# Kernel tuning notes

Hardware: AMD Instinct MI355X
Metric: run time of the kernel (lower is better)

The kernel has to match this reference:

```python
import jax, jax.numpy as jnp
import numpy as np

B, S, D, H = 8, 1024, 1024, 16
DH = D // H  # per-head dim = 64
SCALE = float(np.sqrt(DH))  # normalize_coeff = sqrt(dim_h_k)


def _ln(x, g, b, eps=1e-5):
    m = jnp.mean(x, axis=-1, keepdims=True)
    v = jnp.mean(jnp.square(x - m), axis=-1, keepdims=True)
    return (x - m) / jnp.sqrt(v + eps) * g + b


def setup_inputs() -> dict:
    key = jax.random.key(0)
    ks = jax.random.split(key, 12)
    w = lambda k, shape: (jax.random.normal(k, shape, dtype=jnp.float32) * 0.02)
    return {
        "X": jax.random.normal(ks[0], (B, S, D), dtype=jnp.float32),
        # stacked per-head projection weights (torch Linear: y = x @ W.T + b -> store as [H, D, DH])
        "Wq": w(ks[1], (H, D, DH)), "bq": jnp.zeros((H, DH), jnp.float32),
        "Wk": w(ks[2], (H, D, DH)), "bk": jnp.zeros((H, DH), jnp.float32),
        "Wv": w(ks[3], (H, D, DH)), "bv": jnp.zeros((H, DH), jnp.float32),
        "pre_g": jnp.ones((D,), jnp.float32), "pre_b": jnp.zeros((D,), jnp.float32),
        "post_g": jnp.ones((D,), jnp.float32), "post_b": jnp.zeros((D,), jnp.float32),
        "W1": w(ks[4], (D, 2 * D)), "b1": jnp.zeros((2 * D,), jnp.float32),
        "ln1_g": jnp.ones((2 * D,), jnp.float32), "ln1_b": jnp.zeros((2 * D,), jnp.float32),
        "W2": w(ks[5], (2 * D, D)), "b2": jnp.zeros((D,), jnp.float32),
        "ln2_g": jnp.ones((D,), jnp.float32), "ln2_b": jnp.zeros((D,), jnp.float32),
    }


def reference(X, Wq, bq, Wk, bk, Wv, bv, pre_g, pre_b, post_g, post_b,
              W1, b1, ln1_g, ln1_b, W2, b2, ln2_g, ln2_b):
    # pre-LN + multi-head attention (all heads batched instead of python loop)
    t = _ln(X, pre_g, pre_b)
    q = jnp.einsum('bsd,hdk->bhsk', t, Wq) + bq[:, None, :]   # [B,H,S,DH]
    k = jnp.einsum('bsd,hdk->bhsk', t, Wk) + bk[:, None, :]
    v = jnp.einsum('bsd,hdk->bhsk', t, Wv) + bv[:, None, :]
    scores = jnp.einsum('bhqd,bhkd->bhqk', q, k) / SCALE       # [B,H,S,S]
    p = jax.nn.softmax(scores, axis=-1)
    o = jnp.einsum('bhqk,bhkd->bhqd', p, v)                    # [B,H,S,DH]
    o = o.transpose(0, 2, 1, 3).reshape(B, S, D)               # concat heads
    X = X + o
    # post-LN + MLP (Linear -> LN -> GELU -> Linear -> LN -> GELU)
    t2 = _ln(X, post_g, post_b)
    h = jax.nn.gelu(_ln(t2 @ W1 + b1, ln1_g, ln1_b), approximate=False)
    h = jax.nn.gelu(_ln(h @ W2 + b2, ln2_g, ln2_b), approximate=False)
    return X + h
```

## Files before the change

kernel.cpp:

```cpp
#include <hip/hip_runtime.h>

typedef __attribute__((ext_vector_type(8))) short s16x8;
typedef __attribute__((ext_vector_type(8))) unsigned short u16x8;
typedef __attribute__((ext_vector_type(4))) unsigned short u16x4;
typedef __attribute__((ext_vector_type(4))) float f32x4;

__device__ __forceinline__ unsigned short f2bf(float f) {
  union { float f; unsigned int u; } v; v.f = f;
  unsigned int r = (v.u + 0x7FFFu + ((v.u >> 16) & 1u)) >> 16;
  return (unsigned short)r;
}
__device__ __forceinline__ float bf2f(unsigned short h) {
  union { unsigned int u; float f; } v; v.u = ((unsigned int)h) << 16;
  return v.f;
}
__device__ __forceinline__ float gelu(float x) {
  return 0.5f * x * (1.f + erff(x * 0.70710678118654752f));
}
__device__ __forceinline__ float fexp2(float x) {
  float r; asm("v_exp_f32 %0, %1" : "=v"(r) : "v"(x)); return r;
}

__device__ __forceinline__ void gld16(const void* g, void* l) {
  __builtin_amdgcn_global_load_lds(
      (const __attribute__((address_space(1))) unsigned int*)g,
      (__attribute__((address_space(3))) unsigned int*)l, 16, 0, 0);
}

__device__ __forceinline__ float blk_sum(float v, float* red, int tid, int nw) {
#pragma unroll
  for (int m = 32; m >= 1; m >>= 1) v += __shfl_xor(v, m);
  __syncthreads();
  if ((tid & 63) == 0) red[tid >> 6] = v;
  __syncthreads();
  float t = 0.f;
  for (int i = 0; i < nw; ++i) t += red[i];
  return t;
}

__global__ __launch_bounds__(256) void k_tr(
    const float* __restrict__ in, unsigned short* __restrict__ out,
    int inRS, int outRS, long inBS, long outBS) {
  __shared__ float t[32][33];
  const float* ip = in + (size_t)blockIdx.z * inBS;
  unsigned short* op = out + (size_t)blockIdx.z * outBS;
  const int r0 = blockIdx.y * 32, c0 = blockIdx.x * 32;
  const int tid = threadIdx.x;
  const int r = tid >> 3, c4 = (tid & 7) * 4;
  const f32x4 v = *(const f32x4*)(ip + (size_t)(r0 + r) * inRS + c0 + c4);
#pragma unroll
  for (int i = 0; i < 4; ++i) t[r][c4 + i] = v[i];
  __syncthreads();
  u16x4 o;
#pragma unroll
  for (int i = 0; i < 4; ++i) o[i] = f2bf(t[c4 + i][r]);
  *(u16x4*)(op + (size_t)(c0 + r) * outRS + r0 + c4) = o;
}

__global__ __launch_bounds__(256) void k_bias3(
    const float* __restrict__ a, const float* __restrict__ b,
    const float* __restrict__ c, float* __restrict__ o) {
  int i = blockIdx.x * 256 + threadIdx.x;
  if (i >= 3072) return;
  o[i] = (i < 1024) ? a[i] : ((i < 2048) ? b[i - 1024] : c[i - 2048]);
}

__global__ __launch_bounds__(256) void k_pre_ln(
    const float* __restrict__ X, const float* __restrict__ g,
    const float* __restrict__ bta, unsigned short* __restrict__ out) {
  __shared__ float red[4];
  const int row = blockIdx.x, tid = threadIdx.x;
  const f32x4 x = *(const f32x4*)(X + (size_t)row * 1024 + tid * 4);
  float s = x[0] + x[1] + x[2] + x[3];
  s = blk_sum(s, red, tid, 4);
  const float mean = s * (1.f / 1024.f);
  f32x4 d;
#pragma unroll
  for (int i = 0; i < 4; ++i) d[i] = x[i] - mean;
  float sq = d[0] * d[0] + d[1] * d[1] + d[2] * d[2] + d[3] * d[3];
  sq = blk_sum(sq, red, tid, 4);
  const float rstd = rsqrtf(sq * (1.f / 1024.f) + 1e-5f);
  const f32x4 gv = *(const f32x4*)(g + tid * 4);
  const f32x4 bv = *(const f32x4*)(bta + tid * 4);
  u16x4 o;
#pragma unroll
  for (int i = 0; i < 4; ++i) o[i] = f2bf(d[i] * rstd * gv[i] + bv[i]);
  *(u16x4*)(out + (size_t)row * 1024 + tid * 4) = o;
}

__global__ __launch_bounds__(256) void k_res_ln(
    const float* __restrict__ X, const unsigned short* __restrict__ attn,
    const float* __restrict__ g, const float* __restrict__ bta,
    float* __restrict__ X1, unsigned short* __restrict__ t2) {
  __shared__ float red[4];
  const int row = blockIdx.x, tid = threadIdx.x;
  const f32x4 x = *(const f32x4*)(X + (size_t)row * 1024 + tid * 4);
  const u16x4 a = *(const u16x4*)(attn + (size_t)row * 1024 + tid * 4);
  f32x4 x1;
#pragma unroll
  for (int i = 0; i < 4; ++i) x1[i] = x[i] + bf2f(a[i]);
  *(f32x4*)(X1 + (size_t)row * 1024 + tid * 4) = x1;
  float s = x1[0] + x1[1] + x1[2] + x1[3];
  s = blk_sum(s, red, tid, 4);
  const float mean = s * (1.f / 1024.f);
  f32x4 d;
#pragma unroll
  for (int i = 0; i < 4; ++i) d[i] = x1[i] - mean;
  float sq = d[0] * d[0] + d[1] * d[1] + d[2] * d[2] + d[3] * d[3];
  sq = blk_sum(sq, red, tid, 4);
  const float rstd = rsqrtf(sq * (1.f / 1024.f) + 1e-5f);
  const f32x4 gv = *(const f32x4*)(g + tid * 4);
  const f32x4 bv = *(const f32x4*)(bta + tid * 4);
  u16x4 o;
#pragma unroll
  for (int i = 0; i < 4; ++i) o[i] = f2bf(d[i] * rstd * gv[i] + bv[i]);
  *(u16x4*)(t2 + (size_t)row * 1024 + tid * 4) = o;
}

__global__ __launch_bounds__(256) void k_ln_gelu(
    const unsigned short* __restrict__ in, const float* __restrict__ g,
    const float* __restrict__ bta, unsigned short* __restrict__ out) {
  __shared__ float red[4];
  const int row = blockIdx.x, tid = threadIdx.x;
  const u16x8 iv = *(const u16x8*)(in + (size_t)row * 2048 + tid * 8);
  float v[8];
  float s = 0.f;
#pragma unroll
  for (int i = 0; i < 8; ++i) { v[i] = bf2f(iv[i]); s += v[i]; }
  s = blk_sum(s, red, tid, 4);
  const float mean = s * (1.f / 2048.f);
  float sq = 0.f;
#pragma unroll
  for (int i = 0; i < 8; ++i) { v[i] -= mean; sq += v[i] * v[i]; }
  sq = blk_sum(sq, red, tid, 4);
  const float rstd = rsqrtf(sq * (1.f / 2048.f) + 1e-5f);
  u16x8 o;
#pragma unroll
  for (int i = 0; i < 8; ++i) {
    float t = v[i] * rstd * g[tid * 8 + i] + bta[tid * 8 + i];
    o[i] = f2bf(gelu(t));
  }
  *(u16x8*)(out + (size_t)row * 2048 + tid * 8) = o;
}

__global__ __launch_bounds__(256) void k_final(
    const unsigned short* __restrict__ in, const float* __restrict__ g,
    const float* __restrict__ bta, float* __restrict__ io) {
  __shared__ float red[4];
  const int row = blockIdx.x, tid = threadIdx.x;
  const u16x4 iv = *(const u16x4*)(in + (size_t)row * 1024 + tid * 4);
  float v[4];
  float s = 0.f;
#pragma unroll
  for (int i = 0; i < 4; ++i) { v[i] = bf2f(iv[i]); s += v[i]; }
  s = blk_sum(s, red, tid, 4);
  const float mean = s * (1.f / 1024.f);
  float sq = 0.f;
#pragma unroll
  for (int i = 0; i < 4; ++i) { v[i] -= mean; sq += v[i] * v[i]; }
  sq = blk_sum(sq, red, tid, 4);
  const float rstd = rsqrtf(sq * (1.f / 1024.f) + 1e-5f);
  const f32x4 gv = *(const f32x4*)(g + tid * 4);
  const f32x4 bv = *(const f32x4*)(bta + tid * 4);
  f32x4 xi = *(const f32x4*)(io + (size_t)row * 1024 + tid * 4);
#pragma unroll
  for (int i = 0; i < 4; ++i)
    xi[i] += gelu(v[i] * rstd * gv[i] + bv[i]);
  *(f32x4*)(io + (size_t)row * 1024 + tid * 4) = xi;
}

__global__ __launch_bounds__(256) void k_gemm(
    const unsigned short* __restrict__ A, const unsigned short* __restrict__ Bt,
    const float* __restrict__ bias, unsigned short* __restrict__ C,
    int M, int N, int K, int vsplit, unsigned short* __restrict__ VtO) {
  __shared__ __align__(16) unsigned short As[128 * 64];
  __shared__ __align__(16) unsigned short Bs[128 * 64];
  const int tid = threadIdx.x;
  const int w = tid >> 6, l = tid & 63;
  const int gx = gridDim.x;
  int flat = blockIdx.y * gx + blockIdx.x;
  const int nwg = gx * gridDim.y;
  if ((nwg & 7) == 0) flat = (flat & 7) * (nwg >> 3) + (flat >> 3);
  const int m0 = (flat / gx) * 128, n0 = (flat % gx) * 128;
  const int wr = (w >> 1) * 64, wc = (w & 1) * 64;
  const f32x4 z4 = {0.f, 0.f, 0.f, 0.f};
  f32x4 acc[4][4];
#pragma unroll
  for (int i = 0; i < 4; ++i)
#pragma unroll
    for (int j = 0; j < 4; ++j) acc[i][j] = z4;

  const int srow = l >> 3, scol = (l & 7) * 8;
  for (int kt = 0; kt < K; kt += 64) {
#pragma unroll
    for (int i = 0; i < 4; ++i) {
      const int u = i * 4 + w;
      const int row = u * 8 + srow;
      gld16(A + (size_t)(m0 + row) * K + kt + scol, As + u * 512 + l * 8);
      gld16(Bt + (size_t)(n0 + row) * K + kt + scol, Bs + u * 512 + l * 8);
    }
    __syncthreads();
#pragma unroll
    for (int ks = 0; ks < 2; ++ks) {
      const int kb = ks * 32 + (l >> 4) * 8;
      s16x8 a[4], b[4];
#pragma unroll
      for (int m = 0; m < 4; ++m)
        a[m] = *(const s16x8*)(As + (wr + m * 16 + (l & 15)) * 64 + kb);
#pragma unroll
      for (int n = 0; n < 4; ++n)
        b[n] = *(const s16x8*)(Bs + (wc + n * 16 + (l & 15)) * 64 + kb);
#pragma unroll
      for (int m = 0; m < 4; ++m)
#pragma unroll
        for (int n = 0; n < 4; ++n)
          acc[m][n] = __builtin_amdgcn_mfma_f32_16x16x32_bf16(a[m], b[n], acc[m][n], 0, 0, 0);
    }
    __syncthreads();
  }
  const int rbase = m0 + wr + ((l >> 4) << 2);
  const int cbase = n0 + wc + (l & 15);
#pragma unroll
  for (int n = 0; n < 4; ++n) {
    const int c = cbase + n * 16;
    const float bb = bias[c];
    if ((n0 + wc + n * 16) < vsplit) {
#pragma unroll
      for (int m = 0; m < 4; ++m)
#pragma unroll
        for (int r = 0; r < 4; ++r)
          C[(size_t)(rbase + m * 16 + r) * N + c] = f2bf(acc[m][n][r] + bb);
    } else {
      const int cc = c - vsplit;
      const int hh = cc >> 6, dd = cc & 63;
#pragma unroll
      for (int m = 0; m < 4; ++m) {
        const int rr = rbase + m * 16;
        u16x4 o;
#pragma unroll
        for (int r = 0; r < 4; ++r) o[r] = f2bf(acc[m][n][r] + bb);
        *(u16x4*)(VtO + ((size_t)((rr >> 10) * 16 + hh)) * 65536 + dd * 1024 + (rr & 1023)) = o;
      }
    }
  }
}

__device__ __forceinline__ int swz(int r, int c) {
  return r * 64 + (c ^ ((r & 7) << 3));
}

__global__ __launch_bounds__(256) void k_attn3(
    const unsigned short* __restrict__ qkv, const unsigned short* __restrict__ Vt,
    unsigned short* __restrict__ O) {
  int bid = blockIdx.x;
  bid = (bid & 7) * 256 + (bid >> 3);
  const int qt = bid & 15, h = (bid >> 4) & 15, b = bid >> 8;
  const int tid = threadIdx.x, w = tid >> 6, l = tid & 63;
  const int arow = l & 15, kcol = (l >> 4) * 8;

  __shared__ __align__(16) unsigned short Kb[2][64 * 64];
  __shared__ __align__(16) unsigned short Vb[2][64 * 64];
  __shared__ __align__(16) unsigned short Ps[4][16 * 64];
  unsigned short* ps = &Ps[w][0];

  const unsigned short* qb = qkv + (size_t)b * 1024 * 3072 + h * 64;
  const unsigned short* kb = qb + 1024;
  const unsigned short* vt = Vt + ((size_t)(b * 16 + h)) * 65536;
  const int q0 = qt * 64 + w * 16;

  s16x8 qa[2];
#pragma unroll
  for (int kh = 0; kh < 2; ++kh)
    qa[kh] = *(const s16x8*)(qb + (size_t)(q0 + arow) * 3072 + kh * 32 + kcol);

  const int srow = tid >> 3;
  const int sce = 8 * ((tid & 7) ^ (srow & 7));
  const int sdst = srow * 64 + (tid & 7) * 8;

#pragma unroll
  for (int i = 0; i < 2; ++i) {
    gld16(kb + (size_t)(i * 32 + srow) * 3072 + sce, Kb[0] + i * 2048 + sdst);
    gld16(vt + (size_t)(i * 32 + srow) * 1024 + sce, Vb[0] + i * 2048 + sdst);
  }
  __syncthreads();

  const f32x4 z4 = {0.f, 0.f, 0.f, 0.f};
  f32x4 oacc[4];
#pragma unroll
  for (int i = 0; i < 4; ++i) oacc[i] = z4;
  float mrun[4], lrun[4];
#pragma unroll
  for (int r = 0; r < 4; ++r) { mrun[r] = -1e30f; lrun[r] = 0.f; }

  const float c2 = 0.125f * 1.44269504088896f;

  for (int kc = 0; kc < 16; ++kc) {
    const int cur = kc & 1;
    if (kc < 15) {
      const int key1 = (kc + 1) * 64;
#pragma unroll
      for (int i = 0; i < 2; ++i) {
        gld16(kb + (size_t)(key1 + i * 32 + srow) * 3072 + sce, Kb[cur ^ 1] + i * 2048 + sdst);
        gld16(vt + (size_t)(i * 32 + srow) * 1024 + key1 + sce, Vb[cur ^ 1] + i * 2048 + sdst);
      }
    }
    f32x4 sacc[4];
#pragma unroll
    for (int t = 0; t < 4; ++t) {
      s16x8 k0 = *(const s16x8*)(Kb[cur] + swz(t * 16 + arow, kcol));
      s16x8 k1 = *(const s16x8*)(Kb[cur] + swz(t * 16 + arow, 32 + kcol));
      f32x4 s = z4;
      s = __builtin_amdgcn_mfma_f32_16x16x32_bf16(qa[0], k0, s, 0, 0, 0);
      s = __builtin_amdgcn_mfma_f32_16x16x32_bf16(qa[1], k1, s, 0, 0, 0);
      sacc[t] = s;
    }
    float ss[4][4];
#pragma unroll
    for (int t = 0; t < 4; ++t)
#pragma unroll
      for (int r = 0; r < 4; ++r) ss[t][r] = sacc[t][r] * c2;

    float nm[4], sc[4], psum[4];
#pragma unroll
    for (int r = 0; r < 4; ++r) {
      float m = fmaxf(fmaxf(ss[0][r], ss[1][r]), fmaxf(ss[2][r], ss[3][r]));
#pragma unroll
      for (int msk = 8; msk >= 1; msk >>= 1) m = fmaxf(m, __shfl_xor(m, msk));
      nm[r] = fmaxf(mrun[r], m);
      sc[r] = fexp2(mrun[r] - nm[r]);
      mrun[r] = nm[r];
      psum[r] = 0.f;
    }
#pragma unroll
    for (int t = 0; t < 4; ++t)
#pragma unroll
      for (int r = 0; r < 4; ++r) {
        float p = fexp2(ss[t][r] - nm[r]);
        psum[r] += p;
        ps[swz(((l >> 4) << 2) + r, t * 16 + arow)] = f2bf(p);
      }
#pragma unroll
    for (int r = 0; r < 4; ++r) {
      float s = psum[r];
#pragma unroll
      for (int msk = 8; msk >= 1; msk >>= 1) s += __shfl_xor(s, msk);
      lrun[r] = lrun[r] * sc[r] + s;
#pragma unroll
      for (int dg = 0; dg < 4; ++dg) oacc[dg][r] *= sc[r];
    }
    s16x8 pa[2];
#pragma unroll
    for (int kh = 0; kh < 2; ++kh)
      pa[kh] = *(const s16x8*)(ps + swz(arow, kh * 32 + kcol));
#pragma unroll
    for (int dg = 0; dg < 4; ++dg) {
      s16x8 v0 = *(const s16x8*)(Vb[cur] + swz(dg * 16 + arow, kcol));
      s16x8 v1 = *(const s16x8*)(Vb[cur] + swz(dg * 16 + arow, 32 + kcol));
      oacc[dg] = __builtin_amdgcn_mfma_f32_16x16x32_bf16(pa[0], v0, oacc[dg], 0, 0, 0);
      oacc[dg] = __builtin_amdgcn_mfma_f32_16x16x32_bf16(pa[1], v1, oacc[dg], 0, 0, 0);
    }
    __syncthreads();
  }

  float inv[4];
#pragma unroll
  for (int r = 0; r < 4; ++r) inv[r] = 1.f / lrun[r];
#pragma unroll
  for (int dg = 0; dg < 4; ++dg)
#pragma unroll
    for (int r = 0; r < 4; ++r) {
      const int row = q0 + ((l >> 4) << 2) + r;
      O[(size_t)(b * 1024 + row) * 1024 + h * 64 + dg * 16 + arow] = f2bf(oacc[dg][r] * inv[r]);
    }
}

extern "C" void kernel_launch(void* const* d_in, const int* in_sizes, int n_in,
                              void* d_out, int out_size, void* d_ws, size_t ws_size,
                              hipStream_t stream) {
  const float* X = (const float*)d_in[0];
  const float* Wq = (const float*)d_in[1];
  const float* bq = (const float*)d_in[2];
  const float* Wk = (const float*)d_in[3];
  const float* bk = (const float*)d_in[4];
  const float* Wv = (const float*)d_in[5];
  const float* bv = (const float*)d_in[6];
  const float* pre_g = (const float*)d_in[7];
  const float* pre_b = (const float*)d_in[8];
  const float* post_g = (const float*)d_in[9];
  const float* post_b = (const float*)d_in[10];
  const float* W1 = (const float*)d_in[11];
  const float* b1 = (const float*)d_in[12];
  const float* ln1_g = (const float*)d_in[13];
  const float* ln1_b = (const float*)d_in[14];
  const float* W2 = (const float*)d_in[15];
  const float* b2 = (const float*)d_in[16];
  const float* ln2_g = (const float*)d_in[17];
  const float* ln2_b = (const float*)d_in[18];
  float* out = (float*)d_out;

  char* ws = (char*)d_ws;
  const size_t MB = (size_t)1 << 20;
  unsigned short* t_bf = (unsigned short*)(ws);
  unsigned short* attn_o = (unsigned short*)(ws);
  unsigned short* mlp2 = (unsigned short*)(ws);
  unsigned short* qkv = (unsigned short*)(ws + 16 * MB);
  unsigned short* mlp1 = (unsigned short*)(ws + 16 * MB);
  unsigned short* Vt = (unsigned short*)(ws + 64 * MB);
  unsigned short* h1 = (unsigned short*)(ws + 48 * MB);
  unsigned short* t2 = (unsigned short*)(ws + 80 * MB);
  unsigned short* Wqkvt = (unsigned short*)(ws + 96 * MB);
  unsigned short* W1t = (unsigned short*)(ws + 102 * MB);
  unsigned short* W2t = (unsigned short*)(ws + 106 * MB);
  float* biasq = (float*)(ws + 110 * MB);

  k_tr<<<dim3(2, 32, 16), 256, 0, stream>>>(Wq, Wqkvt, 64, 1024, 65536, 65536);
  k_tr<<<dim3(2, 32, 16), 256, 0, stream>>>(Wk, Wqkvt + 1048576, 64, 1024, 65536, 65536);
  k_tr<<<dim3(2, 32, 16), 256, 0, stream>>>(Wv, Wqkvt + 2097152, 64, 1024, 65536, 65536);
  k_tr<<<dim3(64, 32, 1), 256, 0, stream>>>(W1, W1t, 2048, 1024, 0, 0);
  k_tr<<<dim3(32, 64, 1), 256, 0, stream>>>(W2, W2t, 1024, 2048, 0, 0);
  k_bias3<<<12, 256, 0, stream>>>(bq, bk, bv, biasq);

  k_pre_ln<<<8192, 256, 0, stream>>>(X, pre_g, pre_b, t_bf);
  k_gemm<<<dim3(24, 64), 256, 0, stream>>>(t_bf, Wqkvt, biasq, qkv, 8192, 3072, 1024, 2048, Vt);
  k_attn3<<<2048, 256, 0, stream>>>(qkv, Vt, attn_o);
  k_res_ln<<<8192, 256, 0, stream>>>(X, attn_o, post_g, post_b, out, t2);
  k_gemm<<<dim3(16, 64), 256, 0, stream>>>(t2, W1t, b1, mlp1, 8192, 2048, 1024, 1 << 30, nullptr);
  k_ln_gelu<<<8192, 256, 0, stream>>>(mlp1, ln1_g, ln1_b, h1);
  k_gemm<<<dim3(8, 64), 256, 0, stream>>>(h1, W2t, b2, mlp2, 8192, 1024, 2048, 1 << 30, nullptr);
  k_final<<<8192, 256, 0, stream>>>(mlp2, ln2_g, ln2_b, out);
}
```

Before: 536.6 us.

## Triple-buffer swizzled 256x128 GEMM and streamline attention softmax bookkeeping

The GEMM becomes a 512-thread, 256x128-tile kernel with three-stage dynamic-LDS buffering. It issues loads two tiles ahead with explicit vmcnt waits, uses an XOR-swizzled LDS layout and raises wave priority around the MFMA block. The aim is to hide global-load latency, cut LDS bank conflicts and halve B-operand traffic per output. Attention folds the softmax scale into Q, computes the row sum via MFMA against a ones vector, and skips rescaling when the running max grows by 8 or less. These changes risk bf16 rounding of the scaled Q, and the large LDS use limits occupancy to one block per CU.

Result: faster. 519.1 us (-3.3%).

```diff
diff --git a/kernel.cpp b/kernel.cpp
--- a/kernel.cpp
+++ b/kernel.cpp
@@ -169,20 +169,20 @@
   *(f32x4*)(io + (size_t)row * 1024 + tid * 4) = xi;
 }
 
-__global__ __launch_bounds__(256) void k_gemm(
+__global__ __launch_bounds__(512) void k_gemm2(
     const unsigned short* __restrict__ A, const unsigned short* __restrict__ Bt,
     const float* __restrict__ bias, unsigned short* __restrict__ C,
     int M, int N, int K, int vsplit, unsigned short* __restrict__ VtO) {
-  __shared__ __align__(16) unsigned short As[128 * 64];
-  __shared__ __align__(16) unsigned short Bs[128 * 64];
+  extern __shared__ __align__(16) unsigned short lds[];
   const int tid = threadIdx.x;
   const int w = tid >> 6, l = tid & 63;
+  const int wm = w >> 1, wn = w & 1;
   const int gx = gridDim.x;
   int flat = blockIdx.y * gx + blockIdx.x;
   const int nwg = gx * gridDim.y;
   if ((nwg & 7) == 0) flat = (flat & 7) * (nwg >> 3) + (flat >> 3);
-  const int m0 = (flat / gx) * 128, n0 = (flat % gx) * 128;
-  const int wr = (w >> 1) * 64, wc = (w & 1) * 64;
+  const int m0 = (flat / gx) * 256, n0 = (flat % gx) * 128;
+
   const f32x4 z4 = {0.f, 0.f, 0.f, 0.f};
   f32x4 acc[4][4];
 #pragma unroll
@@ -190,41 +190,75 @@
 #pragma unroll
     for (int j = 0; j < 4; ++j) acc[i][j] = z4;
 
-  const int srow = l >> 3, scol = (l & 7) * 8;
-  for (int kt = 0; kt < K; kt += 64) {
-#pragma unroll
-    for (int i = 0; i < 4; ++i) {
-      const int u = i * 4 + w;
-      const int row = u * 8 + srow;
-      gld16(A + (size_t)(m0 + row) * K + kt + scol, As + u * 512 + l * 8);
-      gld16(Bt + (size_t)(n0 + row) * K + kt + scol, Bs + u * 512 + l * 8);
+#define STAGE_G2(t, d)                                                              \
+  {                                                                                 \
+    const int kb = (t) * 64;                                                        \
+    _Pragma("unroll") for (int i = 0; i < 4; ++i) {                                 \
+      const int s = i * 512 + tid;                                                  \
+      const int row = s >> 3, cs = s & 7;                                           \
+      gld16(A + (size_t)(m0 + row) * K + kb + ((cs ^ (row & 7)) << 3),              \
+            lds + (d) * 24576 + s * 8);                                             \
+    }                                                                               \
+    _Pragma("unroll") for (int i = 0; i < 2; ++i) {                                 \
+      const int s = i * 512 + tid;                                                  \
+      const int row = s >> 3, cs = s & 7;                                           \
+      gld16(Bt + (size_t)(n0 + row) * K + kb + ((cs ^ (row & 7)) << 3),             \
+            lds + (d) * 24576 + 16384 + s * 8);                                     \
+    }                                                                               \
+  }
+
+  const int nt = K >> 6;
+  STAGE_G2(0, 0);
+  STAGE_G2(1, 1);
+
+  for (int t = 0; t < nt; ++t) {
+    const int d = t % 3;
+    if (t + 2 < nt) {
+      const int d2 = (t + 2) % 3;
+      STAGE_G2(t + 2, d2);
+      asm volatile("s_waitcnt vmcnt(12)" ::: "memory");
+    } else if (t + 1 < nt) {
+      asm volatile("s_waitcnt vmcnt(6)" ::: "memory");
+    } else {
+      asm volatile("s_waitcnt vmcnt(0)" ::: "memory");
     }
     __syncthreads();
+
+    const unsigned short* Ab = lds + d * 24576;
+    const unsigned short* Bb = Ab + 16384;
+    __builtin_amdgcn_s_setprio(1);
 #pragma unroll
     for (int ks = 0; ks < 2; ++ks) {
-      const int kb = ks * 32 + (l >> 4) * 8;
+      const int cs = ks * 4 + (l >> 4);
       s16x8 a[4], b[4];
 #pragma unroll
-      for (int m = 0; m < 4; ++m)
-        a[m] = *(const s16x8*)(As + (wr + m * 16 + (l & 15)) * 64 + kb);
-#pragma unroll
-      for (int n = 0; n < 4; ++n)
-        b[n] = *(const s16x8*)(Bs + (wc + n * 16 + (l & 15)) * 64 + kb);
+      for (int m = 0; m < 4; ++m) {
+        const int row = wm * 64 + m * 16 + (l & 15);
+        a[m] = *(const s16x8*)(Ab + row * 64 + ((cs ^ (row & 7)) << 3));
+      }
+#pragma unroll
+      for (int n = 0; n < 4; ++n) {
+        const int row = wn * 64 + n * 16 + (l & 15);
+        b[n] = *(const s16x8*)(Bb + row * 64 + ((cs ^ (row & 7)) << 3));
+      }
 #pragma unroll
       for (int m = 0; m < 4; ++m)
 #pragma unroll
         for (int n = 0; n < 4; ++n)
           acc[m][n] = __builtin_amdgcn_mfma_f32_16x16x32_bf16(a[m], b[n], acc[m][n], 0, 0, 0);
     }
+    __builtin_amdgcn_s_setprio(0);
     __syncthreads();
   }
-  const int rbase = m0 + wr + ((l >> 4) << 2);
-  const int cbase = n0 + wc + (l & 15);
+#undef STAGE_G2
+
+  const int rbase = m0 + wm * 64 + ((l >> 4) << 2);
+  const int cbase = n0 + wn * 64 + (l & 15);
 #pragma unroll
   for (int n = 0; n < 4; ++n) {
     const int c = cbase + n * 16;
     const float bb = bias[c];
-    if ((n0 + wc + n * 16) < vsplit) {
+    if ((n0 + wn * 64 + n * 16) < vsplit) {
 #pragma unroll
       for (int m = 0; m < 4; ++m)
 #pragma unroll
@@ -268,10 +302,20 @@
   const unsigned short* vt = Vt + ((size_t)(b * 16 + h)) * 65536;
   const int q0 = qt * 64 + w * 16;
 
+  const float c2 = 0.125f * 1.44269504088896f;
+
   s16x8 qa[2];
 #pragma unroll
-  for (int kh = 0; kh < 2; ++kh)
-    qa[kh] = *(const s16x8*)(qb + (size_t)(q0 + arow) * 3072 + kh * 32 + kcol);
+  for (int kh = 0; kh < 2; ++kh) {
+    s16x8 q = *(const s16x8*)(qb + (size_t)(q0 + arow) * 3072 + kh * 32 + kcol);
+#pragma unroll
+    for (int j = 0; j < 8; ++j)
+      q[j] = (short)f2bf(bf2f((unsigned short)q[j]) * c2);
+    qa[kh] = q;
+  }
+  s16x8 ones;
+#pragma unroll
+  for (int j = 0; j < 8; ++j) ones[j] = (short)0x3F80;
 
   const int srow = tid >> 3;
   const int sce = 8 * ((tid & 7) ^ (srow & 7));
@@ -288,11 +332,10 @@
   f32x4 oacc[4];
 #pragma unroll
   for (int i = 0; i < 4; ++i) oacc[i] = z4;
-  float mrun[4], lrun[4];
-#pragma unroll
-  for (int r = 0; r < 4; ++r) { mrun[r] = -1e30f; lrun[r] = 0.f; }
-
-  const float c2 = 0.125f * 1.44269504088896f;
+  f32x4 lacc = z4;
+  float mrun[4];
+#pragma unroll
+  for (int r = 0; r < 4; ++r) mrun[r] = -1e30f;
 
   for (int kc = 0; kc < 16; ++kc) {
     const int cur = kc & 1;
@@ -314,44 +357,44 @@
       s = __builtin_amdgcn_mfma_f32_16x16x32_bf16(qa[1], k1, s, 0, 0, 0);
       sacc[t] = s;
     }
-    float ss[4][4];
+    float rmax[4];
+#pragma unroll
+    for (int r = 0; r < 4; ++r) {
+      float m = fmaxf(fmaxf(sacc[0][r], sacc[1][r]), fmaxf(sacc[2][r], sacc[3][r]));
+#pragma unroll
+      for (int msk = 8; msk >= 1; msk >>= 1) m = fmaxf(m, __shfl_xor(m, msk));
+      rmax[r] = m;
+    }
+    const float need = fmaxf(fmaxf(rmax[0] - mrun[0], rmax[1] - mrun[1]),
+                             fmaxf(rmax[2] - mrun[2], rmax[3] - mrun[3]));
+    if (!__all(need <= 8.f)) {
+      float sc[4];
+#pragma unroll
+      for (int r = 0; r < 4; ++r) {
+        const float nm = fmaxf(mrun[r], rmax[r]);
+        sc[r] = fexp2(mrun[r] - nm);
+        mrun[r] = nm;
+      }
+#pragma unroll
+      for (int r = 0; r < 4; ++r) {
+        lacc[r] *= sc[r];
+#pragma unroll
+        for (int dg = 0; dg < 4; ++dg) oacc[dg][r] *= sc[r];
+      }
+    }
 #pragma unroll
     for (int t = 0; t < 4; ++t)
 #pragma unroll
-      for (int r = 0; r < 4; ++r) ss[t][r] = sacc[t][r] * c2;
-
-    float nm[4], sc[4], psum[4];
-#pragma unroll
-    for (int r = 0; r < 4; ++r) {
-      float m = fmaxf(fmaxf(ss[0][r], ss[1][r]), fmaxf(ss[2][r], ss[3][r]));
-#pragma unroll
-      for (int msk = 8; msk >= 1; msk >>= 1) m = fmaxf(m, __shfl_xor(m, msk));
-      nm[r] = fmaxf(mrun[r], m);
-      sc[r] = fexp2(mrun[r] - nm[r]);
-      mrun[r] = nm[r];
-      psum[r] = 0.f;
-    }
-#pragma unroll
-    for (int t = 0; t < 4; ++t)
-#pragma unroll
       for (int r = 0; r < 4; ++r) {
-        float p = fexp2(ss[t][r] - nm[r]);
-        psum[r] += p;
+        const float p = fexp2(sacc[t][r] - mrun[r]);
         ps[swz(((l >> 4) << 2) + r, t * 16 + arow)] = f2bf(p);
       }
-#pragma unroll
-    for (int r = 0; r < 4; ++r) {
-      float s = psum[r];
-#pragma unroll
-      for (int msk = 8; msk >= 1; msk >>= 1) s += __shfl_xor(s, msk);
-      lrun[r] = lrun[r] * sc[r] + s;
-#pragma unroll
-      for (int dg = 0; dg < 4; ++dg) oacc[dg][r] *= sc[r];
-    }
     s16x8 pa[2];
 #pragma unroll
     for (int kh = 0; kh < 2; ++kh)
       pa[kh] = *(const s16x8*)(ps + swz(arow, kh * 32 + kcol));
+    lacc = __builtin_amdgcn_mfma_f32_16x16x32_bf16(pa[0], ones, lacc, 0, 0, 0);
+    lacc = __builtin_amdgcn_mfma_f32_16x16x32_bf16(pa[1], ones, lacc, 0, 0, 0);
 #pragma unroll
     for (int dg = 0; dg < 4; ++dg) {
       s16x8 v0 = *(const s16x8*)(Vb[cur] + swz(dg * 16 + arow, kcol));
@@ -364,7 +407,7 @@
 
   float inv[4];
 #pragma unroll
-  for (int r = 0; r < 4; ++r) inv[r] = 1.f / lrun[r];
+  for (int r = 0; r < 4; ++r) inv[r] = 1.f / lacc[r];
 #pragma unroll
   for (int dg = 0; dg < 4; ++dg)
 #pragma unroll
@@ -413,6 +456,9 @@
   unsigned short* W2t = (unsigned short*)(ws + 106 * MB);
   float* biasq = (float*)(ws + 110 * MB);
 
+  hipFuncSetAttribute((const void*)k_gemm2,
+                      hipFuncAttributeMaxDynamicSharedMemorySize, 3 * 49152);
+
   k_tr<<<dim3(2, 32, 16), 256, 0, stream>>>(Wq, Wqkvt, 64, 1024, 65536, 65536);
   k_tr<<<dim3(2, 32, 16), 256, 0, stream>>>(Wk, Wqkvt + 1048576, 64, 1024, 65536, 65536);
   k_tr<<<dim3(2, 32, 16), 256, 0, stream>>>(Wv, Wqkvt + 2097152, 64, 1024, 65536, 65536);
@@ -421,11 +467,11 @@
   k_bias3<<<12, 256, 0, stream>>>(bq, bk, bv, biasq);
 
   k_pre_ln<<<8192, 256, 0, stream>>>(X, pre_g, pre_b, t_bf);
-  k_gemm<<<dim3(24, 64), 256, 0, stream>>>(t_bf, Wqkvt, biasq, qkv, 8192, 3072, 1024, 2048, Vt);
+  k_gemm2<<<dim3(24, 32), 512, 3 * 49152, stream>>>(t_bf, Wqkvt, biasq, qkv, 8192, 3072, 1024, 2048, Vt);
   k_attn3<<<2048, 256, 0, stream>>>(qkv, Vt, attn_o);
   k_res_ln<<<8192, 256, 0, stream>>>(X, attn_o, post_g, post_b, out, t2);
-  k_gemm<<<dim3(16, 64), 256, 0, stream>>>(t2, W1t, b1, mlp1, 8192, 2048, 1024, 1 << 30, nullptr);
+  k_gemm2<<<dim3(16, 32), 512, 3 * 49152, stream>>>(t2, W1t, b1, mlp1, 8192, 2048, 1024, 1 << 30, nullptr);
   k_ln_gelu<<<8192, 256, 0, stream>>>(mlp1, ln1_g, ln1_b, h1);
-  k_gemm<<<dim3(8, 64), 256, 0, stream>>>(h1, W2t, b2, mlp2, 8192, 1024, 2048, 1 << 30, nullptr);
+  k_gemm2<<<dim3(8, 32), 512, 3 * 49152, stream>>>(h1, W2t, b2, mlp2, 8192, 1024, 2048, 1 << 30, nullptr);
   k_final<<<8192, 256, 0, stream>>>(mlp2, ln2_g, ln2_b, out);
 }
```
